# Performance work log

Hardware: AMD Instinct MI355X
Metric: run time of the kernel (lower is better)

Reference implementation:

```python
import jax, jax.numpy as jnp
import numpy as np

BATCH = 2
SEQ = 2048          # seq_nodes
DIM = 512
VOCAB = 32000
WINDOW = 4          # s_window default
TOPK = 4            # route_topk / expanded_topk / compressed_topk default
STAGE_LAYERS = (2, 2, 1)                      # lite / mid / full
ALPHAS = ((0.3, 0.25, 0.15), (0.65, 0.55, 0.35), (1.0, 0.9, 0.8))  # (alpha_b, beta_s_to_b, beta_b_to_s)
NEXP = (2151, 2253, 2458)                     # ceil(seq_nodes * expand_ratio)
NCMP = (1844, 1639, 1434)                     # ceil(seq_nodes * compress_ratio)
S_DELTA, B_DELTA, X_DELTA = 0.25, 0.2, 0.15   # s/b/cross delta scales
NLAYERS = sum(STAGE_LAYERS)


def _layernorm(x, g, b, eps=1e-5):
    mu = x.mean(-1, keepdims=True)
    var = ((x - mu) ** 2).mean(-1, keepdims=True)
    return (x - mu) * jax.lax.rsqrt(var + eps) * g + b


def _topk_attend(dst_state, src_state, src_val, w, k):
    # diagonal-bilinear route scores: [b, Ndst, Nsrc]
    scores = jnp.einsum('bnd,bsd->bns', dst_state * w, src_state)
    top_v, top_i = jax.lax.top_k(scores, k)            # sparse top-k routing
    p = jax.nn.softmax(top_v, axis=-1)                 # [b, Ndst, k]
    gs = jax.vmap(lambda s, i: s[i])(src_state, top_i)  # [b, Ndst, k, d]
    gv = jax.vmap(lambda v, i: v[i])(src_val, top_i)
    d_state = jnp.einsum('bnk,bnkd->bnd', p, gs)
    d_val = jnp.einsum('bnk,bnkd->bnd', p, gv)
    return d_state, d_val


def _window_prop(state, val, w, window):
    # causal window-sparse diagonal-bilinear propagation: dst i attends src i-1..i-window
    S = state.shape[1]
    sh_s = jnp.stack([jnp.pad(state, ((0, 0), (k, 0), (0, 0)))[:, :S] for k in range(1, window + 1)], axis=2)
    sh_v = jnp.stack([jnp.pad(val, ((0, 0), (k, 0), (0, 0)))[:, :S] for k in range(1, window + 1)], axis=2)
    scores = jnp.einsum('bsd,bswd->bsw', state * w, sh_s)
    mask = jnp.arange(S)[:, None] >= jnp.arange(1, window + 1)[None, :]
    p = jax.nn.softmax(jnp.where(mask, scores, -1e9), axis=-1) * mask
    return jnp.einsum('bsw,bswd->bsd', p, sh_s), jnp.einsum('bsw,bswd->bsd', p, sh_v)


def setup_inputs() -> dict:
    key = jax.random.key(0)
    ks = iter(jax.random.split(key, 32))
    f32 = jnp.float32
    inp = {
        'tokens': jax.random.randint(next(ks), (BATCH, SEQ), 0, VOCAB),
        'embed': 0.02 * jax.random.normal(next(ks), (VOCAB, DIM), f32),
        'readout_w': 0.02 * jax.random.normal(next(ks), (DIM, VOCAB), f32),
        'readout_b': jnp.zeros((VOCAB,), f32),
        'w_s': 0.05 * jax.random.normal(next(ks), (NLAYERS, DIM), f32),
        'w_se': 0.05 * jax.random.normal(next(ks), (NLAYERS, DIM), f32),
        'w_sc': 0.05 * jax.random.normal(next(ks), (NLAYERS, DIM), f32),
        'w_s2e': 0.05 * jax.random.normal(next(ks), (NLAYERS, DIM), f32),
        'w_e2s': 0.05 * jax.random.normal(next(ks), (NLAYERS, DIM), f32),
        'w_s2c': 0.05 * jax.random.normal(next(ks), (NLAYERS, DIM), f32),
        'w_c2s': 0.05 * jax.random.normal(next(ks), (NLAYERS, DIM), f32),
        'ln_s_g': jnp.ones((NLAYERS, DIM), f32), 'ln_s_b': jnp.zeros((NLAYERS, DIM), f32),
        'ln_e_g': jnp.ones((NLAYERS, DIM), f32), 'ln_e_b': jnp.zeros((NLAYERS, DIM), f32),
        'ln_c_g': jnp.ones((NLAYERS, DIM), f32), 'ln_c_b': jnp.zeros((NLAYERS, DIM), f32),
    }
    for st in range(3):
        inp[f'pe_e{st}'] = 0.02 * jax.random.normal(next(ks), (NEXP[st], DIM), f32)
        inp[f'pe_c{st}'] = 0.02 * jax.random.normal(next(ks), (NCMP[st], DIM), f32)
    return inp


def reference(tokens, embed, readout_w, readout_b, w_s, w_se, w_sc, w_s2e, w_e2s, w_s2c, w_c2s,
              ln_s_g, ln_s_b, ln_e_g, ln_e_b, ln_c_g, ln_c_b,
              pe_e0, pe_e1, pe_e2, pe_c0, pe_c1, pe_c2):
    pe_e = (pe_e0, pe_e1, pe_e2)
    pe_c = (pe_c0, pe_c1, pe_c2)
    x = embed[tokens]                    # [b, S, d]
    s_state, s_val = x, x
    li = 0
    B = tokens.shape[0]
    for st in range(3):
        alpha, bs2b, bb2s = ALPHAS[st]
        e_state = jnp.broadcast_to(pe_e[st], (B,) + pe_e[st].shape); e_val = e_state
        c_state = jnp.broadcast_to(pe_c[st], (B,) + pe_c[st].shape); c_val = c_state
        for _ in range(STAGE_LAYERS[st]):
            # sequence window propagation
            ds, dv = _window_prop(s_state, s_val, w_s[li], WINDOW)
            s_state = s_state + S_DELTA * ds; s_val = s_val + S_DELTA * dv
            # S -> expanded / compressed top-k transitions
            ds, dv = _topk_attend(e_state, s_state, s_val, w_s2e[li], TOPK)
            e_state = e_state + X_DELTA * bs2b * alpha * ds; e_val = e_val + X_DELTA * bs2b * alpha * dv
            ds, dv = _topk_attend(c_state, s_state, s_val, w_s2c[li], TOPK)
            c_state = c_state + X_DELTA * bs2b * alpha * ds; c_val = c_val + X_DELTA * bs2b * alpha * dv
            # B self top-k propagation
            ds, dv = _topk_attend(e_state, e_state, e_val, w_se[li], TOPK)
            e_state = e_state + B_DELTA * alpha * ds; e_val = e_val + B_DELTA * alpha * dv
            ds, dv = _topk_attend(c_state, c_state, c_val, w_sc[li], TOPK)
            c_state = c_state + B_DELTA * alpha * ds; c_val = c_val + B_DELTA * alpha * dv
            # B -> S top-k transitions
            ds1, dv1 = _topk_attend(s_state, e_state, e_val, w_e2s[li], TOPK)
            ds2, dv2 = _topk_attend(s_state, c_state, c_val, w_c2s[li], TOPK)
            s_state = s_state + X_DELTA * bb2s * (ds1 + ds2)
            s_val = s_val + X_DELTA * bb2s * (dv1 + dv2)
            # stabilize: tanh state, layernorm values (norm_position='post')
            s_state = jnp.tanh(s_state); s_val = _layernorm(s_val, ln_s_g[li], ln_s_b[li])
            e_state = jnp.tanh(e_state); e_val = _layernorm(e_val, ln_e_g[li], ln_e_b[li])
            c_state = jnp.tanh(c_state); c_val = _layernorm(c_val, ln_c_g[li], ln_c_b[li])
            li += 1
    return s_val @ readout_w + readout_b   # [b, S, vocab]
```

## Files before the change

### kernel.cpp

```cpp
#include <hip/hip_runtime.h>
#include <hip/hip_bf16.h>
#include <math.h>

#define DIM 512
#define SEQ 2048
#define NB 2
#define NEG_INF (-1e30f)

typedef __bf16 bf16x8 __attribute__((ext_vector_type(8)));
typedef float f32x4 __attribute__((ext_vector_type(4)));

static __device__ __forceinline__ float wave_sum(float x) {
#pragma unroll
  for (int off = 32; off; off >>= 1) x += __shfl_xor(x, off, 64);
  return x;
}

static __device__ __forceinline__ bf16x8 pack8(float4 a, float4 b) {
  bf16x8 r;
  r[0] = (__bf16)a.x; r[1] = (__bf16)a.y; r[2] = (__bf16)a.z; r[3] = (__bf16)a.w;
  r[4] = (__bf16)b.x; r[5] = (__bf16)b.y; r[6] = (__bf16)b.z; r[7] = (__bf16)b.w;
  return r;
}

static __device__ __forceinline__ float4 mul4(float4 a, float4 b) {
  return make_float4(a.x * b.x, a.y * b.y, a.z * b.z, a.w * b.w);
}

static __device__ __forceinline__ void gload16(const void* g, void* l) {
  __builtin_amdgcn_global_load_lds((const __attribute__((address_space(1))) void*)g,
                                   (__attribute__((address_space(3))) void*)l, 16, 0, 0);
}

__global__ __launch_bounds__(128) void k_embed(const int* __restrict__ tok,
                                               const float* __restrict__ emb,
                                               float* __restrict__ sS,
                                               float* __restrict__ sV) {
  long row = blockIdx.x;
  int t = tok[row];
  const float4* src = (const float4*)(emb + (long)t * DIM);
  float4* a = (float4*)(sS + row * DIM);
  float4* b = (float4*)(sV + row * DIM);
  int i = threadIdx.x;
  float4 v = src[i];
  a[i] = v;
  b[i] = v;
}

__global__ __launch_bounds__(256) void k_bcast2(const float* __restrict__ pe,
                                                float* __restrict__ s, float* __restrict__ v,
                                                __bf16* __restrict__ mb,
                                                const float* __restrict__ wA,
                                                __bf16* __restrict__ awbOut,
                                                int N, int Npad) {
  int wid = threadIdx.x >> 6, lane = threadIdx.x & 63;
  long row = (long)blockIdx.x * 4 + wid;
  if (row >= (long)NB * Npad) return;
  int b = (int)(row / Npad), m = (int)(row % Npad);
  int d0 = lane * 8;
  if (m < N) {
    float4 x0 = *(const float4*)(pe + (long)m * DIM + d0);
    float4 x1 = *(const float4*)(pe + (long)m * DIM + d0 + 4);
    long fo = ((long)b * N + m) * DIM + d0;
    *(float4*)(s + fo) = x0; *(float4*)(s + fo + 4) = x1;
    *(float4*)(v + fo) = x0; *(float4*)(v + fo + 4) = x1;
    *(bf16x8*)(mb + row * DIM + d0) = pack8(x0, x1);
    float4 w0 = *(const float4*)(wA + d0);
    float4 w1 = *(const float4*)(wA + d0 + 4);
    *(bf16x8*)(awbOut + row * DIM + d0) = pack8(mul4(x0, w0), mul4(x1, w1));
  } else {
    bf16x8 z;
#pragma unroll
    for (int i = 0; i < 8; ++i) z[i] = (__bf16)0.f;
    *(bf16x8*)(mb + row * DIM + d0) = z;
    *(bf16x8*)(awbOut + row * DIM + d0) = z;
  }
}

__global__ __launch_bounds__(256) void k_transpose_rw(const float* __restrict__ in,
                                                      __bf16* __restrict__ out) {
  __shared__ float t[32][33];
  int tx = threadIdx.x, ty = threadIdx.y;
  int n0 = blockIdx.x * 32, k0 = blockIdx.y * 32;
#pragma unroll
  for (int i = 0; i < 4; ++i)
    t[ty + i * 8][tx] = in[(long)(k0 + ty + i * 8) * 32000 + n0 + tx];
  __syncthreads();
#pragma unroll
  for (int i = 0; i < 4; ++i)
    out[(long)(n0 + ty + i * 8) * DIM + k0 + tx] = (__bf16)t[tx][ty + i * 8];
}

__global__ __launch_bounds__(256) void k_window(const float* __restrict__ sS,
                                                const float* __restrict__ sV,
                                                const float* __restrict__ w,
                                                float* __restrict__ oS,
                                                float* __restrict__ oV,
                                                __bf16* __restrict__ oSb,
                                                const float* __restrict__ wE,
                                                const float* __restrict__ wC,
                                                __bf16* __restrict__ awbE,
                                                __bf16* __restrict__ awbC) {
  int wid = threadIdx.x >> 6, lane = threadIdx.x & 63;
  long row = (long)blockIdx.x * 4 + wid;
  int i = (int)(row & (SEQ - 1));
  int d0 = lane * 8;
  const float* ps = sS + row * DIM + d0;
  const float* pv = sV + row * DIM + d0;
  float4 s0 = *(const float4*)ps;
  float4 s1 = *(const float4*)(ps + 4);
  float4 w0 = *(const float4*)(w + d0);
  float4 w1 = *(const float4*)(w + d0 + 4);
  float4 aw0 = mul4(s0, w0);
  float4 aw1 = mul4(s1, w1);
  float4 nS0[4], nS1[4], nV0[4], nV1[4];
  float sc[4];
#pragma unroll
  for (int k = 0; k < 4; ++k) {
    bool valid = (i >= k + 1);
    const float* qs = ps - (long)(k + 1) * DIM;
    const float* qv = pv - (long)(k + 1) * DIM;
    if (valid) {
      nS0[k] = *(const float4*)qs;
      nS1[k] = *(const float4*)(qs + 4);
      nV0[k] = *(const float4*)qv;
      nV1[k] = *(const float4*)(qv + 4);
    } else {
      nS0[k] = make_float4(0.f, 0.f, 0.f, 0.f);
      nS1[k] = nS0[k]; nV0[k] = nS0[k]; nV1[k] = nS0[k];
    }
    sc[k] = aw0.x * nS0[k].x + aw0.y * nS0[k].y + aw0.z * nS0[k].z + aw0.w * nS0[k].w +
            aw1.x * nS1[k].x + aw1.y * nS1[k].y + aw1.z * nS1[k].z + aw1.w * nS1[k].w;
  }
#pragma unroll
  for (int k = 0; k < 4; ++k) sc[k] = wave_sum(sc[k]);
  float m = NEG_INF;
#pragma unroll
  for (int k = 0; k < 4; ++k)
    if (i >= k + 1 && sc[k] > m) m = sc[k];
  float p[4];
  float Z = 0.f;
#pragma unroll
  for (int k = 0; k < 4; ++k) {
    p[k] = (i >= k + 1) ? expf(sc[k] - m) : 0.f;
    Z += p[k];
  }
  float invZ = (Z > 0.f) ? (1.f / Z) : 0.f;
  float4 v0 = *(const float4*)pv;
  float4 v1 = *(const float4*)(pv + 4);
  float4 os0 = s0, os1 = s1, ov0 = v0, ov1 = v1;
#pragma unroll
  for (int k = 0; k < 4; ++k) {
    float c = 0.25f * p[k] * invZ;
    os0.x += c * nS0[k].x; os0.y += c * nS0[k].y; os0.z += c * nS0[k].z; os0.w += c * nS0[k].w;
    os1.x += c * nS1[k].x; os1.y += c * nS1[k].y; os1.z += c * nS1[k].z; os1.w += c * nS1[k].w;
    ov0.x += c * nV0[k].x; ov0.y += c * nV0[k].y; ov0.z += c * nV0[k].z; ov0.w += c * nV0[k].w;
    ov1.x += c * nV1[k].x; ov1.y += c * nV1[k].y; ov1.z += c * nV1[k].z; ov1.w += c * nV1[k].w;
  }
  *(float4*)(oS + row * DIM + d0) = os0;
  *(float4*)(oS + row * DIM + d0 + 4) = os1;
  *(float4*)(oV + row * DIM + d0) = ov0;
  *(float4*)(oV + row * DIM + d0 + 4) = ov1;
  *(bf16x8*)(oSb + row * DIM + d0) = pack8(os0, os1);
  float4 we0 = *(const float4*)(wE + d0);
  float4 we1 = *(const float4*)(wE + d0 + 4);
  *(bf16x8*)(awbE + row * DIM + d0) = pack8(mul4(os0, we0), mul4(os1, we1));
  float4 wc0 = *(const float4*)(wC + d0);
  float4 wc1 = *(const float4*)(wC + d0 + 4);
  *(bf16x8*)(awbC + row * DIM + d0) = pack8(mul4(os0, wc0), mul4(os1, wc1));
}

__global__ __launch_bounds__(256) void k_mfma_nt2(const __bf16* __restrict__ A,
                                                  const __bf16* __restrict__ Bm,
                                                  float* __restrict__ C,
                                                  int Mpad, int Npad, int ldc) {
  __shared__ __align__(1024) char lds[32768];
  const int tid = threadIdx.x;
  const int wid = tid >> 6, lane = tid & 63;
  const int b = blockIdx.z;
  const long m0 = (long)blockIdx.y * 128;
  const long n0 = (long)blockIdx.x * 128;
  const char* Ab = (const char*)(A + ((long)b * Mpad + m0) * DIM);
  const char* Bb = (const char*)(Bm + ((long)b * Npad + n0) * DIM);
  const int mw = (wid >> 1) * 64, nw = (wid & 1) * 64;

  int srow[2], scol[2], dofs[2];
#pragma unroll
  for (int is = 0; is < 2; ++is) {
    int d = is * 4096 + wid * 1024 + lane * 16;
    int s = d ^ (((d >> 8) & 3) << 4);
    srow[is] = s >> 6;
    scol[is] = s & 63;
    dofs[is] = is * 4096 + wid * 1024;
  }
  int aoff[4], boff[4];
#pragma unroll
  for (int f = 0; f < 4; ++f) {
    int rowA = mw + f * 16 + (lane & 15);
    int byA = rowA * 64 + (lane >> 4) * 16;
    aoff[f] = byA ^ (((byA >> 8) & 3) << 4);
    int rowB = nw + f * 16 + (lane & 15);
    int byB = rowB * 64 + (lane >> 4) * 16;
    boff[f] = (byB ^ (((byB >> 8) & 3) << 4)) + 8192;
  }
  auto stage = [&](int buf, int k0) {
#pragma unroll
    for (int is = 0; is < 2; ++is) {
      gload16(Ab + (long)srow[is] * (DIM * 2) + k0 * 2 + scol[is], lds + buf * 16384 + dofs[is]);
      gload16(Bb + (long)srow[is] * (DIM * 2) + k0 * 2 + scol[is], lds + buf * 16384 + 8192 + dofs[is]);
    }
  };

  f32x4 acc[4][4] = {};
  stage(0, 0);
  asm volatile("s_waitcnt vmcnt(0)" ::: "memory");
  __syncthreads();
  int cur = 0;
  for (int k0 = 0; k0 < DIM; k0 += 32) {
    const bool more = (k0 + 32 < DIM);
    if (more) stage(cur ^ 1, k0 + 32);
    const char* base = lds + cur * 16384;
    bf16x8 af[4], bf[4];
#pragma unroll
    for (int f = 0; f < 4; ++f) {
      af[f] = *(const bf16x8*)(base + aoff[f]);
      bf[f] = *(const bf16x8*)(base + boff[f]);
    }
#pragma unroll
    for (int i = 0; i < 4; ++i)
#pragma unroll
      for (int j = 0; j < 4; ++j)
        acc[i][j] = __builtin_amdgcn_mfma_f32_16x16x32_bf16(af[i], bf[j], acc[i][j], 0, 0, 0);
    if (more) {
      asm volatile("s_waitcnt vmcnt(0)" ::: "memory");
      __syncthreads();
      cur ^= 1;
    }
  }
  float* Cb = C + ((long)b * Mpad + m0) * ldc + n0;
#pragma unroll
  for (int i = 0; i < 4; ++i) {
    int mrow = mw + i * 16 + (lane >> 4) * 4;
#pragma unroll
    for (int r = 0; r < 4; ++r) {
      long moff = (long)(mrow + r) * ldc;
#pragma unroll
      for (int j = 0; j < 4; ++j) {
        int ncol = nw + j * 16 + (lane & 15);
        Cb[moff + ncol] = acc[i][j][r];
      }
    }
  }
}

__global__ __launch_bounds__(256) void k_mfma_ro(const __bf16* __restrict__ A,
                                                 const __bf16* __restrict__ Bm,
                                                 float* __restrict__ C,
                                                 const float* __restrict__ bias,
                                                 int Mpad, int Npad, int ldc) {
  __shared__ __align__(1024) char lds[32768];
  const int tid = threadIdx.x;
  const int wid = tid >> 6, lane = tid & 63;
  const long m0 = (long)blockIdx.x * 128;
  const long n0 = (long)blockIdx.y * 128;
  const char* Ab = (const char*)(A + m0 * DIM);
  const char* Bb = (const char*)(Bm + n0 * DIM);
  const int mw = (wid >> 1) * 64, nw = (wid & 1) * 64;

  int srow[2], scol[2], dofs[2];
#pragma unroll
  for (int is = 0; is < 2; ++is) {
    int d = is * 4096 + wid * 1024 + lane * 16;
    int s = d ^ (((d >> 8) & 3) << 4);
    srow[is] = s >> 6;
    scol[is] = s & 63;
    dofs[is] = is * 4096 + wid * 1024;
  }
  int aoff[4], boff[4];
#pragma unroll
  for (int f = 0; f < 4; ++f) {
    int rowA = mw + f * 16 + (lane & 15);
    int byA = rowA * 64 + (lane >> 4) * 16;
    aoff[f] = byA ^ (((byA >> 8) & 3) << 4);
    int rowB = nw + f * 16 + (lane & 15);
    int byB = rowB * 64 + (lane >> 4) * 16;
    boff[f] = (byB ^ (((byB >> 8) & 3) << 4)) + 8192;
  }
  auto stage = [&](int buf, int k0) {
#pragma unroll
    for (int is = 0; is < 2; ++is) {
      gload16(Ab + (long)srow[is] * (DIM * 2) + k0 * 2 + scol[is], lds + buf * 16384 + dofs[is]);
      gload16(Bb + (long)srow[is] * (DIM * 2) + k0 * 2 + scol[is], lds + buf * 16384 + 8192 + dofs[is]);
    }
  };

  f32x4 acc[4][4] = {};
  stage(0, 0);
  asm volatile("s_waitcnt vmcnt(0)" ::: "memory");
  __syncthreads();
  int cur = 0;
  for (int k0 = 0; k0 < DIM; k0 += 32) {
    const bool more = (k0 + 32 < DIM);
    if (more) stage(cur ^ 1, k0 + 32);
    const char* base = lds + cur * 16384;
    bf16x8 af[4], bf[4];
#pragma unroll
    for (int f = 0; f < 4; ++f) {
      af[f] = *(const bf16x8*)(base + aoff[f]);
      bf[f] = *(const bf16x8*)(base + boff[f]);
    }
#pragma unroll
    for (int i = 0; i < 4; ++i)
#pragma unroll
      for (int j = 0; j < 4; ++j)
        acc[i][j] = __builtin_amdgcn_mfma_f32_16x16x32_bf16(af[i], bf[j], acc[i][j], 0, 0, 0);
    if (more) {
      asm volatile("s_waitcnt vmcnt(0)" ::: "memory");
      __syncthreads();
      cur ^= 1;
    }
  }
  float* Cb = C + m0 * ldc + n0;
  float bv[4];
#pragma unroll
  for (int j = 0; j < 4; ++j) bv[j] = bias[n0 + nw + j * 16 + (lane & 15)];
#pragma unroll
  for (int i = 0; i < 4; ++i) {
    int mrow = mw + i * 16 + (lane >> 4) * 4;
#pragma unroll
    for (int r = 0; r < 4; ++r) {
      long moff = (long)(mrow + r) * ldc;
#pragma unroll
      for (int j = 0; j < 4; ++j) {
        int ncol = nw + j * 16 + (lane & 15);
        __builtin_nontemporal_store(acc[i][j][r] + bv[j], &Cb[moff + ncol]);
      }
    }
  }
}

__global__ __launch_bounds__(256) void k_topk_update(
    const float* __restrict__ scores, int Mpad, int ldc,
    const float* __restrict__ srcS, const float* __restrict__ srcV,
    const float* __restrict__ baseS, const float* __restrict__ baseV,
    float* __restrict__ outS, float* __restrict__ outV,
    __bf16* __restrict__ outSb, int MpadMir,
    const float* __restrict__ wNext, __bf16* __restrict__ outAw,
    const float* __restrict__ lnG, const float* __restrict__ lnB,
    __bf16* __restrict__ outValb,
    int M, int N, float scale) {
  int wid = threadIdx.x >> 6, lane = threadIdx.x & 63;
  long row = (long)blockIdx.x * 4 + wid;
  long total = (long)NB * M;
  if (row >= total) return;
  int b = (int)(row / M);
  int m = (int)(row - (long)b * M);
  const float* sc = scores + ((long)b * Mpad + m) * ldc;
  float v0 = NEG_INF, v1 = NEG_INF, v2 = NEG_INF, v3 = NEG_INF;
  int i0 = 0x7fffffff, i1 = 0x7fffffff, i2 = 0x7fffffff, i3 = 0x7fffffff;
  for (int s = lane; s < N; s += 64) {
    float x = sc[s];
    if (x > v3) {
      if (x > v0) { v3 = v2; i3 = i2; v2 = v1; i2 = i1; v1 = v0; i1 = i0; v0 = x; i0 = s; }
      else if (x > v1) { v3 = v2; i3 = i2; v2 = v1; i2 = i1; v1 = x; i1 = s; }
      else if (x > v2) { v3 = v2; i3 = i2; v2 = x; i2 = s; }
      else { v3 = x; i3 = s; }
    }
  }
  int ptr = 0;
  float rv[4];
  int ri[4];
#pragma unroll
  for (int r = 0; r < 4; ++r) {
    float cv = (ptr == 0) ? v0 : (ptr == 1) ? v1 : (ptr == 2) ? v2 : (ptr == 3) ? v3 : NEG_INF;
    int ci = (ptr == 0) ? i0 : (ptr == 1) ? i1 : (ptr == 2) ? i2 : (ptr == 3) ? i3 : 0x7fffffff;
    float bv = cv;
    int bi = ci;
#pragma unroll
    for (int off = 32; off; off >>= 1) {
      float ov = __shfl_xor(bv, off, 64);
      int oi = __shfl_xor(bi, off, 64);
      if (ov > bv || (ov == bv && oi < bi)) { bv = ov; bi = oi; }
    }
    rv[r] = bv;
    ri[r] = bi;
    if (bi == ci) ptr++;
  }
  float p0 = 1.f, p1 = expf(rv[1] - rv[0]), p2 = expf(rv[2] - rv[0]), p3 = expf(rv[3] - rv[0]);
  float invZ = 1.f / (p0 + p1 + p2 + p3);
  p0 *= invZ; p1 *= invZ; p2 *= invZ; p3 *= invZ;
  int d0 = lane * 8;
  long sb = (long)b * N;
  const float* gs0 = srcS + (sb + ri[0]) * DIM + d0;
  const float* gs1 = srcS + (sb + ri[1]) * DIM + d0;
  const float* gs2 = srcS + (sb + ri[2]) * DIM + d0;
  const float* gs3 = srcS + (sb + ri[3]) * DIM + d0;
  const float* gv0 = srcV + (sb + ri[0]) * DIM + d0;
  const float* gv1 = srcV + (sb + ri[1]) * DIM + d0;
  const float* gv2 = srcV + (sb + ri[2]) * DIM + d0;
  const float* gv3 = srcV + (sb + ri[3]) * DIM + d0;
  long ro = row * DIM + d0;
  float4 osv[2], qsv[2];
#pragma unroll
  for (int h = 0; h < 2; ++h) {
    float4 x0 = *(const float4*)(gs0 + h * 4);
    float4 x1 = *(const float4*)(gs1 + h * 4);
    float4 x2 = *(const float4*)(gs2 + h * 4);
    float4 x3 = *(const float4*)(gs3 + h * 4);
    float4 o = *(const float4*)(baseS + ro + h * 4);
    o.x += scale * (p0 * x0.x + p1 * x1.x + p2 * x2.x + p3 * x3.x);
    o.y += scale * (p0 * x0.y + p1 * x1.y + p2 * x2.y + p3 * x3.y);
    o.z += scale * (p0 * x0.z + p1 * x1.z + p2 * x2.z + p3 * x3.z);
    o.w += scale * (p0 * x0.w + p1 * x1.w + p2 * x2.w + p3 * x3.w);
    osv[h] = o;
    float4 y0 = *(const float4*)(gv0 + h * 4);
    float4 y1 = *(const float4*)(gv1 + h * 4);
    float4 y2 = *(const float4*)(gv2 + h * 4);
    float4 y3 = *(const float4*)(gv3 + h * 4);
    float4 q = *(const float4*)(baseV + ro + h * 4);
    q.x += scale * (p0 * y0.x + p1 * y1.x + p2 * y2.x + p3 * y3.x);
    q.y += scale * (p0 * y0.y + p1 * y1.y + p2 * y2.y + p3 * y3.y);
    q.z += scale * (p0 * y0.z + p1 * y1.z + p2 * y2.z + p3 * y3.z);
    q.w += scale * (p0 * y0.w + p1 * y1.w + p2 * y2.w + p3 * y3.w);
    qsv[h] = q;
  }
  if (lnG) {
    osv[0].x = tanhf(osv[0].x); osv[0].y = tanhf(osv[0].y);
    osv[0].z = tanhf(osv[0].z); osv[0].w = tanhf(osv[0].w);
    osv[1].x = tanhf(osv[1].x); osv[1].y = tanhf(osv[1].y);
    osv[1].z = tanhf(osv[1].z); osv[1].w = tanhf(osv[1].w);
    float sum = qsv[0].x + qsv[0].y + qsv[0].z + qsv[0].w +
                qsv[1].x + qsv[1].y + qsv[1].z + qsv[1].w;
    sum = wave_sum(sum);
    float mu = sum * (1.f / DIM);
    float d[8] = {qsv[0].x - mu, qsv[0].y - mu, qsv[0].z - mu, qsv[0].w - mu,
                  qsv[1].x - mu, qsv[1].y - mu, qsv[1].z - mu, qsv[1].w - mu};
    float ss = d[0]*d[0] + d[1]*d[1] + d[2]*d[2] + d[3]*d[3] +
               d[4]*d[4] + d[5]*d[5] + d[6]*d[6] + d[7]*d[7];
    ss = wave_sum(ss);
    float rs = rsqrtf(ss * (1.f / DIM) + 1e-5f);
    float4 g0 = *(const float4*)(lnG + d0);
    float4 g1 = *(const float4*)(lnG + d0 + 4);
    float4 b0 = *(const float4*)(lnB + d0);
    float4 b1 = *(const float4*)(lnB + d0 + 4);
    qsv[0].x = d[0] * rs * g0.x + b0.x; qsv[0].y = d[1] * rs * g0.y + b0.y;
    qsv[0].z = d[2] * rs * g0.z + b0.z; qsv[0].w = d[3] * rs * g0.w + b0.w;
    qsv[1].x = d[4] * rs * g1.x + b1.x; qsv[1].y = d[5] * rs * g1.y + b1.y;
    qsv[1].z = d[6] * rs * g1.z + b1.z; qsv[1].w = d[7] * rs * g1.w + b1.w;
  }
#pragma unroll
  for (int h = 0; h < 2; ++h) {
    *(float4*)(outS + ro + h * 4) = osv[h];
    *(float4*)(outV + ro + h * 4) = qsv[h];
  }
  if (outSb) {
    *(bf16x8*)(outSb + ((long)b * MpadMir + m) * DIM + d0) = pack8(osv[0], osv[1]);
  }
  if (outAw) {
    float4 w0 = *(const float4*)(wNext + d0);
    float4 w1 = *(const float4*)(wNext + d0 + 4);
    *(bf16x8*)(outAw + ((long)b * MpadMir + m) * DIM + d0) =
        pack8(mul4(osv[0], w0), mul4(osv[1], w1));
  }
  if (outValb) {
    *(bf16x8*)(outValb + ro) = pack8(qsv[0], qsv[1]);
  }
}

__global__ __launch_bounds__(256) void k_stab(float* __restrict__ state,
                                              float* __restrict__ val,
                                              const float* __restrict__ g,
                                              const float* __restrict__ beta,
                                              const float* __restrict__ wNext,
                                              __bf16* __restrict__ awbOut,
                                              int M, int Mpad) {
  int wid = threadIdx.x >> 6, lane = threadIdx.x & 63;
  long row = (long)blockIdx.x * 4 + wid;
  if (row >= (long)NB * M) return;
  int d0 = lane * 8;
  float* ps = state + row * DIM + d0;
  float4 s0 = *(float4*)ps;
  float4 s1 = *(float4*)(ps + 4);
  s0.x = tanhf(s0.x); s0.y = tanhf(s0.y); s0.z = tanhf(s0.z); s0.w = tanhf(s0.w);
  s1.x = tanhf(s1.x); s1.y = tanhf(s1.y); s1.z = tanhf(s1.z); s1.w = tanhf(s1.w);
  *(float4*)ps = s0;
  *(float4*)(ps + 4) = s1;
  float* pv = val + row * DIM + d0;
  float4 x0 = *(float4*)pv;
  float4 x1 = *(float4*)(pv + 4);
  float sum = x0.x + x0.y + x0.z + x0.w + x1.x + x1.y + x1.z + x1.w;
  sum = wave_sum(sum);
  float mu = sum * (1.f / DIM);
  float d[8] = {x0.x - mu, x0.y - mu, x0.z - mu, x0.w - mu,
                x1.x - mu, x1.y - mu, x1.z - mu, x1.w - mu};
  float ss = d[0]*d[0] + d[1]*d[1] + d[2]*d[2] + d[3]*d[3] + d[4]*d[4] + d[5]*d[5] + d[6]*d[6] + d[7]*d[7];
  ss = wave_sum(ss);
  float rs = rsqrtf(ss * (1.f / DIM) + 1e-5f);
  float4 g0 = *(const float4*)(g + d0);
  float4 g1 = *(const float4*)(g + d0 + 4);
  float4 b0 = *(const float4*)(beta + d0);
  float4 b1 = *(const float4*)(beta + d0 + 4);
  x0.x = d[0] * rs * g0.x + b0.x; x0.y = d[1] * rs * g0.y + b0.y;
  x0.z = d[2] * rs * g0.z + b0.z; x0.w = d[3] * rs * g0.w + b0.w;
  x1.x = d[4] * rs * g1.x + b1.x; x1.y = d[5] * rs * g1.y + b1.y;
  x1.z = d[6] * rs * g1.z + b1.z; x1.w = d[7] * rs * g1.w + b1.w;
  *(float4*)pv = x0;
  *(float4*)(pv + 4) = x1;
  if (awbOut) {
    int b = (int)(row / M);
    int m = (int)(row - (long)b * M);
    float4 w0 = *(const float4*)(wNext + d0);
    float4 w1 = *(const float4*)(wNext + d0 + 4);
    *(bf16x8*)(awbOut + ((long)b * Mpad + m) * DIM + d0) =
        pack8(mul4(s0, w0), mul4(s1, w1));
  }
}

extern "C" void kernel_launch(void* const* d_in, const int* in_sizes, int n_in,
                              void* d_out, int out_size, void* d_ws, size_t ws_size,
                              hipStream_t stream) {
  (void)in_sizes; (void)n_in; (void)out_size; (void)ws_size;
  const int* tokens = (const int*)d_in[0];
  const float* embed = (const float*)d_in[1];
  const float* readout_w = (const float*)d_in[2];
  const float* readout_b = (const float*)d_in[3];
  const float* w_s = (const float*)d_in[4];
  const float* w_se = (const float*)d_in[5];
  const float* w_sc = (const float*)d_in[6];
  const float* w_s2e = (const float*)d_in[7];
  const float* w_e2s = (const float*)d_in[8];
  const float* w_s2c = (const float*)d_in[9];
  const float* w_c2s = (const float*)d_in[10];
  const float* ln_s_g = (const float*)d_in[11];
  const float* ln_s_b = (const float*)d_in[12];
  const float* ln_e_g = (const float*)d_in[13];
  const float* ln_e_b = (const float*)d_in[14];
  const float* ln_c_g = (const float*)d_in[15];
  const float* ln_c_b = (const float*)d_in[16];
  const float* pe_e[3] = {(const float*)d_in[17], (const float*)d_in[19], (const float*)d_in[21]};
  const float* pe_c[3] = {(const float*)d_in[18], (const float*)d_in[20], (const float*)d_in[22]};

  static const int NEXP[3] = {2151, 2253, 2458};
  static const int NCMP[3] = {1844, 1639, 1434};
  static const int NEXP_P[3] = {2176, 2304, 2560};
  static const int NCMP_P[3] = {1920, 1664, 1536};
  static const int LAYERS[3] = {2, 2, 1};
  static const float ALPHA[3][3] = {{0.3f, 0.25f, 0.15f}, {0.65f, 0.55f, 0.35f}, {1.0f, 0.9f, 0.8f}};

  const long SZ_S = 2L * SEQ * DIM;
  const long SZ_E = 2L * 2458 * DIM;
  const long SZ_C = 2L * 1844 * DIM;
  float* ws = (float*)d_ws;
  float* sS[2] = {ws, ws + SZ_S}; ws += 2 * SZ_S;
  float* sV[2] = {ws, ws + SZ_S}; ws += 2 * SZ_S;
  float* eS[2] = {ws, ws + SZ_E}; ws += 2 * SZ_E;
  float* eV[2] = {ws, ws + SZ_E}; ws += 2 * SZ_E;
  float* cS[2] = {ws, ws + SZ_C}; ws += 2 * SZ_C;
  float* cV[2] = {ws, ws + SZ_C}; ws += 2 * SZ_C;
  float* scores = ws; ws += 2L * 2560 * 2560;
  __bf16* bw = (__bf16*)ws;
  __bf16* sb = bw;      bw += 2L * 2048 * DIM;
  __bf16* eb = bw;      bw += 2L * 2560 * DIM;
  __bf16* cb = bw;      bw += 2L * 1920 * DIM;
  __bf16* awbS2e = bw;  bw += 2L * 2560 * DIM;
  __bf16* awbS2c = bw;  bw += 2L * 1920 * DIM;
  __bf16* awbSe = bw;   bw += 2L * 2560 * DIM;
  __bf16* awbSc = bw;   bw += 2L * 1920 * DIM;
  __bf16* awbE = bw;    bw += 2L * 2048 * DIM;
  __bf16* awbC = bw;    bw += 2L * 2048 * DIM;
  __bf16* valb = bw;    bw += 4096L * DIM;
  __bf16* rwT = bw;     bw += 32000L * DIM;

  auto cdiv = [](long a, long b) { return (int)((a + b - 1) / b); };

  k_embed<<<NB * SEQ, 128, 0, stream>>>(tokens, embed, sS[0], sV[0]);

  int cs = 0, li = 0;
  for (int st = 0; st < 3; ++st) {
    const int Ne = NEXP[st], Nc = NCMP[st];
    const int NeP = NEXP_P[st], NcP = NCMP_P[st];
    const float alpha = ALPHA[st][0], bs2b = ALPHA[st][1], bb2s = ALPHA[st][2];
    const float sc_x = 0.15f * bs2b * alpha;
    const float sc_b = 0.2f * alpha;
    const float sc_s = 0.15f * bb2s;
    int ce = 0, cc = 0;
    k_bcast2<<<cdiv((long)NB * NeP, 4), 256, 0, stream>>>(
        pe_e[st], eS[0], eV[0], eb, w_s2e + (long)li * DIM, awbS2e, Ne, NeP);
    k_bcast2<<<cdiv((long)NB * NcP, 4), 256, 0, stream>>>(
        pe_c[st], cS[0], cV[0], cb, w_s2c + (long)li * DIM, awbS2c, Nc, NcP);
    for (int l = 0; l < LAYERS[st]; ++l) {
      const bool lastOfStage = (l == LAYERS[st] - 1);
      const bool finalLayer = (st == 2);
      k_window<<<NB * SEQ / 4, 256, 0, stream>>>(
          sS[cs], sV[cs], w_s + (long)li * DIM, sS[cs ^ 1], sV[cs ^ 1], sb,
          w_e2s + (long)li * DIM, w_c2s + (long)li * DIM, awbE, awbC);
      cs ^= 1;
      {
        dim3 g(SEQ / 128, NeP / 128, NB);
        k_mfma_nt2<<<g, 256, 0, stream>>>(awbS2e, sb, scores, NeP, SEQ, SEQ);
      }
      k_topk_update<<<cdiv((long)NB * Ne, 4), 256, 0, stream>>>(
          scores, NeP, SEQ, sS[cs], sV[cs], eS[ce], eV[ce], eS[ce ^ 1], eV[ce ^ 1],
          eb, NeP, w_se + (long)li * DIM, awbSe, nullptr, nullptr, nullptr, Ne, SEQ, sc_x);
      ce ^= 1;
      {
        dim3 g(SEQ / 128, NcP / 128, NB);
        k_mfma_nt2<<<g, 256, 0, stream>>>(awbS2c, sb, scores, NcP, SEQ, SEQ);
      }
      k_topk_update<<<cdiv((long)NB * Nc, 4), 256, 0, stream>>>(
          scores, NcP, SEQ, sS[cs], sV[cs], cS[cc], cV[cc], cS[cc ^ 1], cV[cc ^ 1],
          cb, NcP, w_sc + (long)li * DIM, awbSc, nullptr, nullptr, nullptr, Nc, SEQ, sc_x);
      cc ^= 1;
      {
        dim3 g(NeP / 128, NeP / 128, NB);
        k_mfma_nt2<<<g, 256, 0, stream>>>(awbSe, eb, scores, NeP, NeP, NeP);
      }
      k_topk_update<<<cdiv((long)NB * Ne, 4), 256, 0, stream>>>(
          scores, NeP, NeP, eS[ce], eV[ce], eS[ce], eV[ce], eS[ce ^ 1], eV[ce ^ 1],
          eb, NeP, nullptr, nullptr, nullptr, nullptr, nullptr, Ne, Ne, sc_b);
      ce ^= 1;
      {
        dim3 g(NcP / 128, NcP / 128, NB);
        k_mfma_nt2<<<g, 256, 0, stream>>>(awbSc, cb, scores, NcP, NcP, NcP);
      }
      k_topk_update<<<cdiv((long)NB * Nc, 4), 256, 0, stream>>>(
          scores, NcP, NcP, cS[cc], cV[cc], cS[cc], cV[cc], cS[cc ^ 1], cV[cc ^ 1],
          cb, NcP, nullptr, nullptr, nullptr, nullptr, nullptr, Nc, Nc, sc_b);
      cc ^= 1;
      {
        dim3 g(NeP / 128, SEQ / 128, NB);
        k_mfma_nt2<<<g, 256, 0, stream>>>(awbE, eb, scores, SEQ, NeP, NeP);
      }
      k_topk_update<<<NB * SEQ / 4, 256, 0, stream>>>(
          scores, SEQ, NeP, eS[ce], eV[ce], sS[cs], sV[cs], sS[cs ^ 1], sV[cs ^ 1],
          nullptr, 0, nullptr, nullptr, nullptr, nullptr, nullptr, SEQ, Ne, sc_s);
      {
        dim3 g(NcP / 128, SEQ / 128, NB);
        k_mfma_nt2<<<g, 256, 0, stream>>>(awbC, cb, scores, SEQ, NcP, NcP);
      }
      k_topk_update<<<NB * SEQ / 4, 256, 0, stream>>>(
          scores, SEQ, NcP, cS[cc], cV[cc], sS[cs ^ 1], sV[cs ^ 1], sS[cs ^ 1], sV[cs ^ 1],
          nullptr, 0, nullptr, nullptr,
          ln_s_g + (long)li * DIM, ln_s_b + (long)li * DIM,
          finalLayer ? valb : nullptr, SEQ, Nc, sc_s);
      cs ^= 1;
      if (!lastOfStage) {
        k_stab<<<cdiv((long)NB * Ne, 4), 256, 0, stream>>>(
            eS[ce], eV[ce], ln_e_g + (long)li * DIM, ln_e_b + (long)li * DIM,
            w_s2e + (long)(li + 1) * DIM, awbS2e, Ne, NeP);
        k_stab<<<cdiv((long)NB * Nc, 4), 256, 0, stream>>>(
            cS[cc], cV[cc], ln_c_g + (long)li * DIM, ln_c_b + (long)li * DIM,
            w_s2c + (long)(li + 1) * DIM, awbS2c, Nc, NcP);
      }
      ++li;
    }
  }
  {
    dim3 g(1000, 16);
    dim3 blk(32, 8);
    k_transpose_rw<<<g, blk, 0, stream>>>(readout_w, rwT);
  }
  {
    dim3 g((NB * SEQ) / 128, 32000 / 128, 1);
    k_mfma_ro<<<g, 256, 0, stream>>>(valb, rwT, (float*)d_out, readout_b, NB * SEQ, 32000, 32000);
  }
}
```

Before: 1.841 ms.

## Batch paired score GEMMs into grouped launches and swizzle readout GEMM tiles

Replaces pairs of independent score GEMMs (S→E and S→C, E-self and C-self, E→S and C→S) with one grouped MFMA kernel whose blockIdx.y selects the problem. Results go to separate regions of an enlarged scores buffer, so each top-k consumer reads its own slice. This cuts launch count and fills the GPU better, since single GEMMs are small relative to the CU count. The readout GEMM also remaps block indices in an XCD-aware strided order to improve L2 locality. The cost is some idle early-exit blocks in the grouped grid and a larger workspace.

```diff
diff --git a/kernel.cpp b/kernel.cpp
--- a/kernel.cpp
+++ b/kernel.cpp
@@ -170,16 +170,28 @@
   *(bf16x8*)(awbC + row * DIM + d0) = pack8(mul4(os0, wc0), mul4(os1, wc1));
 }
 
-__global__ __launch_bounds__(256) void k_mfma_nt2(const __bf16* __restrict__ A,
-                                                  const __bf16* __restrict__ Bm,
-                                                  float* __restrict__ C,
-                                                  int Mpad, int Npad, int ldc) {
+__global__ __launch_bounds__(256) void k_mfma_g2(
+    const __bf16* __restrict__ A1, const __bf16* __restrict__ B1, float* __restrict__ C1,
+    int Mpad1, int Npad1, int ldc1,
+    const __bf16* __restrict__ A2, const __bf16* __restrict__ B2, float* __restrict__ C2,
+    int Mpad2, int Npad2, int ldc2) {
+  const __bf16* A; const __bf16* Bm; float* C;
+  int Mpad, Npad, ldc;
+  long my;
+  int M1b = Mpad1 >> 7;
+  if ((int)blockIdx.y < M1b) {
+    A = A1; Bm = B1; C = C1; Mpad = Mpad1; Npad = Npad1; ldc = ldc1; my = blockIdx.y;
+  } else {
+    A = A2; Bm = B2; C = C2; Mpad = Mpad2; Npad = Npad2; ldc = ldc2; my = blockIdx.y - M1b;
+  }
+  const long n0 = (long)blockIdx.x * 128;
+  if (n0 >= Npad) return;
+  const long m0 = my * 128;
+
   __shared__ __align__(1024) char lds[32768];
   const int tid = threadIdx.x;
   const int wid = tid >> 6, lane = tid & 63;
   const int b = blockIdx.z;
-  const long m0 = (long)blockIdx.y * 128;
-  const long n0 = (long)blockIdx.x * 128;
   const char* Ab = (const char*)(A + ((long)b * Mpad + m0) * DIM);
   const char* Bb = (const char*)(Bm + ((long)b * Npad + n0) * DIM);
   const int mw = (wid >> 1) * 64, nw = (wid & 1) * 64;
@@ -261,8 +273,12 @@
   __shared__ __align__(1024) char lds[32768];
   const int tid = threadIdx.x;
   const int wid = tid >> 6, lane = tid & 63;
-  const long m0 = (long)blockIdx.x * 128;
-  const long n0 = (long)blockIdx.y * 128;
+  long hw = (long)blockIdx.y * gridDim.x + blockIdx.x;
+  long nwg = (long)gridDim.x * gridDim.y;
+  long cpx = nwg >> 3;
+  long l = (hw & 7) * cpx + (hw >> 3);
+  const long m0 = (l % gridDim.x) * 128;
+  const long n0 = (l / gridDim.x) * 128;
   const char* Ab = (const char*)(A + m0 * DIM);
   const char* Bb = (const char*)(Bm + n0 * DIM);
   const int mw = (wid >> 1) * 64, nw = (wid & 1) * 64;
@@ -557,7 +573,7 @@
   float* eV[2] = {ws, ws + SZ_E}; ws += 2 * SZ_E;
   float* cS[2] = {ws, ws + SZ_C}; ws += 2 * SZ_C;
   float* cV[2] = {ws, ws + SZ_C}; ws += 2 * SZ_C;
-  float* scores = ws; ws += 2L * 2560 * 2560;
+  float* scores = ws; ws += 18000000;
   __bf16* bw = (__bf16*)ws;
   __bf16* sb = bw;      bw += 2L * 2048 * DIM;
   __bf16* eb = bw;      bw += 2L * 2560 * DIM;
@@ -595,51 +611,45 @@
           sS[cs], sV[cs], w_s + (long)li * DIM, sS[cs ^ 1], sV[cs ^ 1], sb,
           w_e2s + (long)li * DIM, w_c2s + (long)li * DIM, awbE, awbC);
       cs ^= 1;
+      float* scores2 = scores + (long)NB * NeP * SEQ;
       {
-        dim3 g(SEQ / 128, NeP / 128, NB);
-        k_mfma_nt2<<<g, 256, 0, stream>>>(awbS2e, sb, scores, NeP, SEQ, SEQ);
+        dim3 g(SEQ / 128, (NeP + NcP) / 128, NB);
+        k_mfma_g2<<<g, 256, 0, stream>>>(awbS2e, sb, scores, NeP, SEQ, SEQ,
+                                         awbS2c, sb, scores2, NcP, SEQ, SEQ);
       }
       k_topk_update<<<cdiv((long)NB * Ne, 4), 256, 0, stream>>>(
           scores, NeP, SEQ, sS[cs], sV[cs], eS[ce], eV[ce], eS[ce ^ 1], eV[ce ^ 1],
           eb, NeP, w_se + (long)li * DIM, awbSe, nullptr, nullptr, nullptr, Ne, SEQ, sc_x);
       ce ^= 1;
-      {
-        dim3 g(SEQ / 128, NcP / 128, NB);
-        k_mfma_nt2<<<g, 256, 0, stream>>>(awbS2c, sb, scores, NcP, SEQ, SEQ);
-      }
       k_topk_update<<<cdiv((long)NB * Nc, 4), 256, 0, stream>>>(
-          scores, NcP, SEQ, sS[cs], sV[cs], cS[cc], cV[cc], cS[cc ^ 1], cV[cc ^ 1],
+          scores2, NcP, SEQ, sS[cs], sV[cs], cS[cc], cV[cc], cS[cc ^ 1], cV[cc ^ 1],
           cb, NcP, w_sc + (long)li * DIM, awbSc, nullptr, nullptr, nullptr, Nc, SEQ, sc_x);
       cc ^= 1;
+      float* scores2b = scores + (long)NB * NeP * NeP;
       {
-        dim3 g(NeP / 128, NeP / 128, NB);
-        k_mfma_nt2<<<g, 256, 0, stream>>>(awbSe, eb, scores, NeP, NeP, NeP);
+        dim3 g(NeP / 128, (NeP + NcP) / 128, NB);
+        k_mfma_g2<<<g, 256, 0, stream>>>(awbSe, eb, scores, NeP, NeP, NeP,
+                                         awbSc, cb, scores2b, NcP, NcP, NcP);
       }
       k_topk_update<<<cdiv((long)NB * Ne, 4), 256, 0, stream>>>(
           scores, NeP, NeP, eS[ce], eV[ce], eS[ce], eV[ce], eS[ce ^ 1], eV[ce ^ 1],
           eb, NeP, nullptr, nullptr, nullptr, nullptr, nullptr, Ne, Ne, sc_b);
       ce ^= 1;
-      {
-        dim3 g(NcP / 128, NcP / 128, NB);
-        k_mfma_nt2<<<g, 256, 0, stream>>>(awbSc, cb, scores, NcP, NcP, NcP);
-      }
       k_topk_update<<<cdiv((long)NB * Nc, 4), 256, 0, stream>>>(
-          scores, NcP, NcP, cS[cc], cV[cc], cS[cc], cV[cc], cS[cc ^ 1], cV[cc ^ 1],
+          scores2b, NcP, NcP, cS[cc], cV[cc], cS[cc], cV[cc], cS[cc ^ 1], cV[cc ^ 1],
           cb, NcP, nullptr, nullptr, nullptr, nullptr, nullptr, Nc, Nc, sc_b);
       cc ^= 1;
+      float* scores2c = scores + (long)NB * SEQ * NeP;
       {
-        dim3 g(NeP / 128, SEQ / 128, NB);
-        k_mfma_nt2<<<g, 256, 0, stream>>>(awbE, eb, scores, SEQ, NeP, NeP);
+        dim3 g(NeP / 128, (2 * SEQ) / 128, NB);
+        k_mfma_g2<<<g, 256, 0, stream>>>(awbE, eb, scores, SEQ, NeP, NeP,
+                                         awbC, cb, scores2c, SEQ, NcP, NcP);
       }
       k_topk_update<<<NB * SEQ / 4, 256, 0, stream>>>(
           scores, SEQ, NeP, eS[ce], eV[ce], sS[cs], sV[cs], sS[cs ^ 1], sV[cs ^ 1],
           nullptr, 0, nullptr, nullptr, nullptr, nullptr, nullptr, SEQ, Ne, sc_s);
-      {
-        dim3 g(NcP / 128, SEQ / 128, NB);
-        k_mfma_nt2<<<g, 256, 0, stream>>>(awbC, cb, scores, SEQ, NcP, NcP);
-      }
       k_topk_update<<<NB * SEQ / 4, 256, 0, stream>>>(
-          scores, SEQ, NcP, cS[cc], cV[cc], sS[cs ^ 1], sV[cs ^ 1], sS[cs ^ 1], sV[cs ^ 1],
+          scores2c, SEQ, NcP, cS[cc], cV[cc], sS[cs ^ 1], sV[cs ^ 1], sS[cs ^ 1], sV[cs ^ 1],
           nullptr, 0, nullptr, nullptr,
           ln_s_g + (long)li * DIM, ln_s_b + (long)li * DIM,
           finalLayer ? valb : nullptr, SEQ, Nc, sc_s);
```

New measurement: 1.831 ms. Within noise of the previous version (-0.5%).
